# Performance work log

Measured on AMD Instinct MI355X. Metric: run time of the kernel, lower is better.

Reference implementation:

```python
import jax, jax.numpy as jnp
import numpy as np

S = 2              # scaling_factor
RBF_RADIUS = 2
RADIUS = S * RBF_RADIUS   # high-res pixel radius = 4
WIN = 3                   # 3x3 candidate window -> K = 9 = MAX_NEIGHBOURS
K = WIN * WIN


def setup_inputs() -> dict:
    key = jax.random.key(0)
    k0, k1, k2, k3, k4, k5, k6 = jax.random.split(key, 7)
    A, n, c, h, w = 4, 4, 3, 256, 256
    sh, sw = S * h, S * w
    alts = jax.random.normal(k0, (A, n, c, h, w), jnp.float32)
    # sub-pixel motion offsets in low-res units; clipped so every output pixel
    # keeps at least one valid neighbor inside the RBF radius
    offsets = jnp.clip(0.5 * jax.random.normal(k1, (A, n, 2, h, w), jnp.float32), -1.0, 1.0)
    qs = jax.random.uniform(k2, (A, n, h, w), jnp.float32, minval=0.1, maxval=1.0)
    o11 = jax.random.uniform(k3, (n, sh, sw), jnp.float32, minval=0.5, maxval=2.0)
    o22 = jax.random.uniform(k4, (n, sh, sw), jnp.float32, minval=0.5, maxval=2.0)
    o12 = jax.random.uniform(k5, (n, sh, sw), jnp.float32, minval=-0.2, maxval=0.2)
    o21 = jax.random.uniform(k6, (n, sh, sw), jnp.float32, minval=-0.2, maxval=0.2)
    return {"alts": alts, "offsets": offsets, "qs": qs,
            "o11": o11, "o12": o12, "o21": o21, "o22": o22}


def reference(alts, offsets, qs, o11, o12, o21, o22):
    A, n, c, h, w = alts.shape
    sh, sw = S * h, S * w
    yy = jnp.arange(sh)
    xx = jnp.arange(sw)
    y0 = yy // S                      # base low-res row for each output row
    x0 = xx // S
    d = jnp.arange(WIN) - WIN // 2
    di, dj = jnp.meshgrid(d, d, indexing="ij")
    di, dj = di.ravel(), dj.ravel()   # (K,)
    rn_raw = y0[:, None, None] + di[None, None, :]   # (sh,1,K)
    cn_raw = x0[None, :, None] + dj[None, None, :]   # (1,sw,K)
    inb = ((rn_raw >= 0) & (rn_raw < h) & (cn_raw >= 0) & (cn_raw < w))  # (sh,sw,K)
    rn = jnp.clip(rn_raw, 0, h - 1)
    cn = jnp.clip(cn_raw, 0, w - 1)
    yy_f = yy.astype(jnp.float32)[None, :, None, None]   # (1,sh,1,1)
    xx_f = xx.astype(jnp.float32)[None, None, :, None]   # (1,1,sw,1)
    rn_f = rn.astype(jnp.float32)
    cn_f = cn.astype(jnp.float32)

    x_out = 0.0
    weights = 0.0
    for a in range(A):   # small fixed number of alternate frames
        off_r = offsets[a][:, 0][:, rn, cn]              # (n,sh,sw,K)
        off_c = offsets[a][:, 1][:, rn, cn]
        pos_r = rn_f * S + off_r * S                     # shifted sample positions (high-res)
        pos_c = cn_f * S + off_c * S
        # neighbor validity: in-bounds grid cell and within RBF radius
        a_neigh = (inb & (jnp.abs(pos_r - yy_f) <= RADIUS)
                       & (jnp.abs(pos_c - xx_f) <= RADIUS)).astype(jnp.float32)
        dy = (pos_r - yy_f) / S                          # displacement in low-res units
        dx = (pos_c - xx_f) / S
        rbf_dist = (dx * dx * o11[..., None] + dx * dy * o12[..., None]
                    + dy * dx * o21[..., None] + dy * dy * o22[..., None])
        rbf_w = jnp.exp(-0.5 * jnp.clip(rbf_dist, 0.0, 20.0))
        q_w = qs[a][:, rn, cn]                           # (n,sh,sw,K)
        wgt = rbf_w * q_w * a_neigh
        weights = weights + jnp.sum(wgt, axis=3)         # (n,sh,sw)
        alt_neigh = alts[a][:, :, rn, cn]                # (n,c,sh,sw,K)
        x_out = x_out + jnp.einsum("ncyxk,nyxk->ncyx", alt_neigh, wgt)
    return x_out / weights[:, None, :, :]
```

## Files before the change

kernel.cpp:

```cpp
#include <hip/hip_runtime.h>


#define AF      4
#define NB      4
#define CH      3
#define H       256
#define W       256
#define SH      512
#define SW      512
#define HW      (H*W)
#define SHW     (SH*SW)
#define RADIUS  4.0f
#define MSCALE  0.18033688011112042f
#define CLHI    14.426950408889634f

typedef float v2f __attribute__((ext_vector_type(2)));

__global__ __launch_bounds__(256) void superresolve_kernel(
    const float* __restrict__ alts,
    const float* __restrict__ offsets,
    const float* __restrict__ qs,
    const float* __restrict__ o11,
    const float* __restrict__ o12,
    const float* __restrict__ o21,
    const float* __restrict__ o22,
    float* __restrict__ out)
{
    __shared__ float red[128 * 17];

    const int tid   = threadIdx.x;
    const int wv    = tid >> 6;
    const int lane  = tid & 63;
    const int fpair = wv >> 1;
    const int pix   = ((wv & 1) << 6) + lane;

    const int bid = blockIdx.x;
    const int swz = (bid & 7) * 256 + (bid >> 3);
    const int P   = swz * 128 + pix;

    const int x0 = P & (W - 1);
    const int y0  = __builtin_amdgcn_readfirstlane((P >> 8) & (H - 1));
    const int nn  = __builtin_amdgcn_readfirstlane(P >> 16);
    const int af0 = __builtin_amdgcn_readfirstlane(fpair << 1);

    const int xL = (x0 > 0) ? x0 - 1 : 0;
    const int xR = (x0 < W - 1) ? x0 + 1 : W - 1;
    const int iL = y0 * W + xL;
    const int iC = y0 * W + x0;
    const int iR = y0 * W + xR;
    const bool bL = (x0 > 0);
    const bool bR = (x0 < W - 1);
    const float f2xL = (float)(2 * xL);
    const float f2xC = (float)(2 * x0);
    const float f2xR = (float)(2 * xR);
    const float xf0  = f2xC;
    const float yf0  = (float)(2 * y0);
    const float INF  = __builtin_inff();

    const int obase = (nn * SH + 2 * y0) * SW + 2 * x0;
    const float2 v11a = *(const float2*)(o11 + obase);
    const float2 v11b = *(const float2*)(o11 + obase + SW);
    const float2 v12a = *(const float2*)(o12 + obase);
    const float2 v12b = *(const float2*)(o12 + obase + SW);
    const float2 v21a = *(const float2*)(o21 + obase);
    const float2 v21b = *(const float2*)(o21 + obase + SW);
    const float2 v22a = *(const float2*)(o22 + obase);
    const float2 v22b = *(const float2*)(o22 + obase + SW);

    v2f m11v[2], m12v[2], m22v[2];
    m11v[0] = (v2f){MSCALE * v11a.x, MSCALE * v11a.y};
    m11v[1] = (v2f){MSCALE * v11b.x, MSCALE * v11b.y};
    m12v[0] = (v2f){MSCALE * (v12a.x + v21a.x), MSCALE * (v12a.y + v21a.y)};
    m12v[1] = (v2f){MSCALE * (v12b.x + v21b.x), MSCALE * (v12b.y + v21b.y)};
    m22v[0] = (v2f){MSCALE * v22a.x, MSCALE * v22a.y};
    m22v[1] = (v2f){MSCALE * v22b.x, MSCALE * v22b.y};

    v2f sumwv[2] = {(v2f){0.f,0.f}, (v2f){0.f,0.f}};
    v2f acc0v[2] = {(v2f){0.f,0.f}, (v2f){0.f,0.f}};
    v2f acc1v[2] = {(v2f){0.f,0.f}, (v2f){0.f,0.f}};
    v2f acc2v[2] = {(v2f){0.f,0.f}, (v2f){0.f,0.f}};

#define COLK(or_, oc_, q_, a0_, a1_, a2_, f2x_, COLB, IS_L, NEED_VY)          \
    {                                                                         \
        const float posr = fmaf(or_, 2.0f, rowf);                             \
        const float dy0v = posr - yf0;                                        \
        const float dy1v = dy0v - 1.0f;                                       \
        const float posc = fmaf(oc_, 2.0f, f2x_);                             \
        const float dx0v = posc - xf0;                                        \
        const float dx1v = dx0v - 1.0f;                                       \
        const v2f dxv = (v2f){dx0v, dx1v};                                    \
        const bool vx1 = IS_L ? (dx1v >= -RADIUS) : true;                     \
        _Pragma("unroll")                                                     \
        for (int sy = 0; sy < 2; ++sy) {                                      \
            const float dyv = sy ? dy1v : dy0v;                               \
            const bool okb = (COLB) && (NEED_VY && sy ? (dy1v >= -RADIUS)     \
                                                      : true);                \
            const v2f u = dxv * m11v[sy] + dyv * m12v[sy];                    \
            v2f dv = dxv * u + (dyv * dyv) * m22v[sy];                        \
            dv = __builtin_elementwise_min(dv, (v2f){CLHI, CLHI});            \
            const float f0 = okb ? dv.x : INF;                                \
            const float f1 = (okb && vx1) ? dv.y : INF;                       \
            const v2f ev  = (v2f){exp2f(-f0), exp2f(-f1)};                    \
            const v2f wv2 = ev * (q_);                                        \
            sumwv[sy] += wv2;                                                 \
            acc0v[sy] += wv2 * (a0_);                                         \
            acc1v[sy] += wv2 * (a1_);                                         \
            acc2v[sy] += wv2 * (a2_);                                         \
        }                                                                     \
    }

    #pragma unroll
    for (int ai = 0; ai < 2; ++ai) {
        const int a = af0 + ai;
        const float* offbR = offsets + (size_t)(a * NB + nn) * 2 * HW;
        const float* offbC = offbR + HW;
        const float* qb    = qs   + (size_t)(a * NB + nn) * HW;
        const float* ab0   = alts + (size_t)(a * NB + nn) * CH * HW;
        const float* ab1   = ab0 + HW;
        const float* ab2   = ab0 + 2 * HW;

        #pragma unroll
        for (int di = -1; di <= 1; ++di) {
            if (di == -1 && y0 == 0) continue;
            if (di == +1 && y0 == H - 1) continue;
            const int ro = di * W;
            const float* pR = offbR + ro;
            const float* pC = offbC + ro;
            const float* pQ = qb + ro;
            const float* p0 = ab0 + ro;
            const float* p1 = ab1 + ro;
            const float* p2 = ab2 + ro;
            const float rowf = (float)(2 * (y0 + di));

            const float orL = pR[iL], orC = pR[iC], orR = pR[iR];
            const float ocL = pC[iL], ocC = pC[iC], ocR = pC[iR];
            const float qL  = pQ[iL], qC  = pQ[iC], qR  = pQ[iR];
            const float aL0 = p0[iL], aC0 = p0[iC], aR0 = p0[iR];
            const float aL1 = p1[iL], aC1 = p1[iC], aR1 = p1[iR];
            const float aL2 = p2[iL], aC2 = p2[iC], aR2 = p2[iR];

            const bool needvy = (di == -1);
            COLK(orL, ocL, qL, aL0, aL1, aL2, f2xL, bL,   true,  needvy)
            COLK(orC, ocC, qC, aC0, aC1, aC2, f2xC, true, false, needvy)
            COLK(orR, ocR, qR, aR0, aR1, aR2, f2xR, bR,   false, needvy)
        }
    }
#undef COLK

    if (fpair == 1) {
        float* r = &red[pix * 17];
        #pragma unroll
        for (int sy = 0; sy < 2; ++sy) {
            r[sy*8+0] = sumwv[sy].x; r[sy*8+1] = sumwv[sy].y;
            r[sy*8+2] = acc0v[sy].x; r[sy*8+3] = acc0v[sy].y;
            r[sy*8+4] = acc1v[sy].x; r[sy*8+5] = acc1v[sy].y;
            r[sy*8+6] = acc2v[sy].x; r[sy*8+7] = acc2v[sy].y;
        }
    }
    __syncthreads();
    if (fpair == 0) {
        const float* r = &red[pix * 17];
        #pragma unroll
        for (int sy = 0; sy < 2; ++sy) {
            sumwv[sy].x += r[sy*8+0]; sumwv[sy].y += r[sy*8+1];
            acc0v[sy].x += r[sy*8+2]; acc0v[sy].y += r[sy*8+3];
            acc1v[sy].x += r[sy*8+4]; acc1v[sy].y += r[sy*8+5];
            acc2v[sy].x += r[sy*8+6]; acc2v[sy].y += r[sy*8+7];
        }
        const size_t ob = (size_t)(nn * CH) * SHW + (size_t)(2 * y0) * SW + 2 * x0;
        #pragma unroll
        for (int sy = 0; sy < 2; ++sy) {
            const v2f inv = (v2f){1.0f / sumwv[sy].x, 1.0f / sumwv[sy].y};
            const v2f r0 = acc0v[sy] * inv;
            const v2f r1 = acc1v[sy] * inv;
            const v2f r2 = acc2v[sy] * inv;
            *(float2*)(out + ob + (size_t)sy * SW)         = make_float2(r0.x, r0.y);
            *(float2*)(out + ob + (size_t)sy * SW + SHW)   = make_float2(r1.x, r1.y);
            *(float2*)(out + ob + (size_t)sy * SW + 2*SHW) = make_float2(r2.x, r2.y);
        }
    }
}

extern "C" void kernel_launch(void* const* d_in, const int* in_sizes, int n_in,
                              void* d_out, int out_size, void* d_ws, size_t ws_size,
                              hipStream_t stream) {
    const float* alts    = (const float*)d_in[0];
    const float* offsets = (const float*)d_in[1];
    const float* qs      = (const float*)d_in[2];
    const float* o11     = (const float*)d_in[3];
    const float* o12     = (const float*)d_in[4];
    const float* o21     = (const float*)d_in[5];
    const float* o22     = (const float*)d_in[6];
    float* out = (float*)d_out;

    const int total_threads = NB * H * W * 2;
    const int block = 256;
    const int grid  = total_threads / block;
    superresolve_kernel<<<grid, block, 0, stream>>>(alts, offsets, qs,
                                                    o11, o12, o21, o22, out);
}
```

Measured before the change: 26.01 us.

## Stage neighbor rows into LDS with float4 loads before compute

Each block now cooperatively loads the 3 rows × 6 planes × 4 frames of input data for its 128-pixel row segment into shared memory using float4 loads plus halo elements, then reads the 3x3 neighbourhood from LDS instead of issuing scattered global loads. Clamped rows and columns are used for the halo. This removes redundant, unvectorised global loads that neighbouring threads repeated. In exchange it adds about 39KB of LDS per block, which may lower occupancy, plus an extra barrier before the reduction reuses the buffer.

```diff
diff --git a/kernel.cpp b/kernel.cpp
--- a/kernel.cpp
+++ b/kernel.cpp
@@ -13,6 +13,7 @@
 #define RADIUS  4.0f
 #define MSCALE  0.18033688011112042f
 #define CLHI    14.426950408889634f
+#define SEGW    136
 
 typedef float v2f __attribute__((ext_vector_type(2)));
 
@@ -26,7 +27,7 @@
     const float* __restrict__ o22,
     float* __restrict__ out)
 {
-    __shared__ float red[128 * 17];
+    __shared__ float lds[72 * SEGW];
 
     const int tid   = threadIdx.x;
     const int wv    = tid >> 6;
@@ -36,26 +37,19 @@
 
     const int bid = blockIdx.x;
     const int swz = (bid & 7) * 256 + (bid >> 3);
-    const int P   = swz * 128 + pix;
-
-    const int x0 = P & (W - 1);
-    const int y0  = __builtin_amdgcn_readfirstlane((P >> 8) & (H - 1));
-    const int nn  = __builtin_amdgcn_readfirstlane(P >> 16);
+
+    const int xbase = (swz & 1) << 7;
+    const int y0  = __builtin_amdgcn_readfirstlane((swz >> 1) & (H - 1));
+    const int nn  = __builtin_amdgcn_readfirstlane(swz >> 9);
     const int af0 = __builtin_amdgcn_readfirstlane(fpair << 1);
-
-    const int xL = (x0 > 0) ? x0 - 1 : 0;
-    const int xR = (x0 < W - 1) ? x0 + 1 : W - 1;
-    const int iL = y0 * W + xL;
-    const int iC = y0 * W + x0;
-    const int iR = y0 * W + xR;
-    const bool bL = (x0 > 0);
-    const bool bR = (x0 < W - 1);
-    const float f2xL = (float)(2 * xL);
-    const float f2xC = (float)(2 * x0);
-    const float f2xR = (float)(2 * xR);
-    const float xf0  = f2xC;
-    const float yf0  = (float)(2 * y0);
-    const float INF  = __builtin_inff();
+    const int x0  = xbase + pix;
+
+    auto plane_ptr = [&](int a, int p) -> const float* {
+        const size_t fb = (size_t)(a * NB + nn);
+        if (p < 2)  return offsets + fb * 2 * HW + (size_t)p * HW;
+        if (p == 2) return qs + fb * HW;
+        return alts + (fb * CH + (size_t)(p - 3)) * HW;
+    };
 
     const int obase = (nn * SH + 2 * y0) * SW + 2 * x0;
     const float2 v11a = *(const float2*)(o11 + obase);
@@ -67,6 +61,34 @@
     const float2 v22a = *(const float2*)(o22 + obase);
     const float2 v22b = *(const float2*)(o22 + obase + SW);
 
+    {
+        const int s0 = tid >> 5;
+        const int j  = tid & 31;
+        #pragma unroll
+        for (int it = 0; it < 9; ++it) {
+            const int s  = it * 8 + s0;
+            const int a  = s / 18;
+            const int pr = s - a * 18;
+            const int p  = pr / 3;
+            const int r  = pr - p * 3;
+            const int row = min(max(y0 + r - 1, 0), H - 1);
+            const float* gp = plane_ptr(a, p) + row * W + xbase + j * 4;
+            const float4 v = *(const float4*)gp;
+            *(float4*)&lds[s * SEGW + 4 + j * 4] = v;
+        }
+        if (tid < 144) {
+            const int s    = tid >> 1;
+            const int side = tid & 1;
+            const int a  = s / 18;
+            const int pr = s - a * 18;
+            const int p  = pr / 3;
+            const int r  = pr - p * 3;
+            const int row = min(max(y0 + r - 1, 0), H - 1);
+            const int gx  = side ? min(xbase + 128, W - 1) : max(xbase - 1, 0);
+            lds[s * SEGW + (side ? 132 : 3)] = plane_ptr(a, p)[row * W + gx];
+        }
+    }
+
     v2f m11v[2], m12v[2], m22v[2];
     m11v[0] = (v2f){MSCALE * v11a.x, MSCALE * v11a.y};
     m11v[1] = (v2f){MSCALE * v11b.x, MSCALE * v11b.y};
@@ -75,10 +97,23 @@
     m22v[0] = (v2f){MSCALE * v22a.x, MSCALE * v22a.y};
     m22v[1] = (v2f){MSCALE * v22b.x, MSCALE * v22b.y};
 
+    const bool bL = (x0 > 0);
+    const bool bR = (x0 < W - 1);
+    const int  xL = bL ? x0 - 1 : 0;
+    const int  xR = bR ? x0 + 1 : W - 1;
+    const float f2xL = (float)(2 * xL);
+    const float f2xC = (float)(2 * x0);
+    const float f2xR = (float)(2 * xR);
+    const float xf0  = f2xC;
+    const float yf0  = (float)(2 * y0);
+    const float INF  = __builtin_inff();
+
     v2f sumwv[2] = {(v2f){0.f,0.f}, (v2f){0.f,0.f}};
     v2f acc0v[2] = {(v2f){0.f,0.f}, (v2f){0.f,0.f}};
     v2f acc1v[2] = {(v2f){0.f,0.f}, (v2f){0.f,0.f}};
     v2f acc2v[2] = {(v2f){0.f,0.f}, (v2f){0.f,0.f}};
+
+    __syncthreads();
 
 #define COLK(or_, oc_, q_, a0_, a1_, a2_, f2x_, COLB, IS_L, NEED_VY)          \
     {                                                                         \
@@ -111,35 +146,27 @@
 
     #pragma unroll
     for (int ai = 0; ai < 2; ++ai) {
-        const int a = af0 + ai;
-        const float* offbR = offsets + (size_t)(a * NB + nn) * 2 * HW;
-        const float* offbC = offbR + HW;
-        const float* qb    = qs   + (size_t)(a * NB + nn) * HW;
-        const float* ab0   = alts + (size_t)(a * NB + nn) * CH * HW;
-        const float* ab1   = ab0 + HW;
-        const float* ab2   = ab0 + 2 * HW;
-
-        #pragma unroll
-        for (int di = -1; di <= 1; ++di) {
-            if (di == -1 && y0 == 0) continue;
-            if (di == +1 && y0 == H - 1) continue;
-            const int ro = di * W;
-            const float* pR = offbR + ro;
-            const float* pC = offbC + ro;
-            const float* pQ = qb + ro;
-            const float* p0 = ab0 + ro;
-            const float* p1 = ab1 + ro;
-            const float* p2 = ab2 + ro;
-            const float rowf = (float)(2 * (y0 + di));
-
-            const float orL = pR[iL], orC = pR[iC], orR = pR[iR];
-            const float ocL = pC[iL], ocC = pC[iC], ocR = pC[iR];
-            const float qL  = pQ[iL], qC  = pQ[iC], qR  = pQ[iR];
-            const float aL0 = p0[iL], aC0 = p0[iC], aR0 = p0[iR];
-            const float aL1 = p1[iL], aC1 = p1[iC], aR1 = p1[iR];
-            const float aL2 = p2[iL], aC2 = p2[iC], aR2 = p2[iR];
-
-            const bool needvy = (di == -1);
+        const int a    = af0 + ai;
+        const int segA = a * 18;
+        #pragma unroll
+        for (int dr = 0; dr < 3; ++dr) {
+            if (dr == 0 && y0 == 0) continue;
+            if (dr == 2 && y0 == H - 1) continue;
+            const float rowf = (float)(2 * (y0 + dr - 1));
+            const int b0 = (segA + dr) * SEGW + 3 + pix;
+            const int b1 = b0 + 3 * SEGW;
+            const int b2 = b0 + 6 * SEGW;
+            const int b3 = b0 + 9 * SEGW;
+            const int b4 = b0 + 12 * SEGW;
+            const int b5 = b0 + 15 * SEGW;
+            const float orL = lds[b0],     orC = lds[b0 + 1], orR = lds[b0 + 2];
+            const float ocL = lds[b1],     ocC = lds[b1 + 1], ocR = lds[b1 + 2];
+            const float qL  = lds[b2],     qC  = lds[b2 + 1], qR  = lds[b2 + 2];
+            const float aL0 = lds[b3],     aC0 = lds[b3 + 1], aR0 = lds[b3 + 2];
+            const float aL1 = lds[b4],     aC1 = lds[b4 + 1], aR1 = lds[b4 + 2];
+            const float aL2 = lds[b5],     aC2 = lds[b5 + 1], aR2 = lds[b5 + 2];
+
+            const bool needvy = (dr == 0);
             COLK(orL, ocL, qL, aL0, aL1, aL2, f2xL, bL,   true,  needvy)
             COLK(orC, ocC, qC, aC0, aC1, aC2, f2xC, true, false, needvy)
             COLK(orR, ocR, qR, aR0, aR1, aR2, f2xR, bR,   false, needvy)
@@ -147,8 +174,9 @@
     }
 #undef COLK
 
+    __syncthreads();
     if (fpair == 1) {
-        float* r = &red[pix * 17];
+        float* r = &lds[pix * 17];
         #pragma unroll
         for (int sy = 0; sy < 2; ++sy) {
             r[sy*8+0] = sumwv[sy].x; r[sy*8+1] = sumwv[sy].y;
@@ -159,7 +187,7 @@
     }
     __syncthreads();
     if (fpair == 0) {
-        const float* r = &red[pix * 17];
+        const float* r = &lds[pix * 17];
         #pragma unroll
         for (int sy = 0; sy < 2; ++sy) {
             sumwv[sy].x += r[sy*8+0]; sumwv[sy].y += r[sy*8+1];
```

Result: slower. 31.10 us (+19.6%).
